# Kernel optimization log

Hardware: AMD Instinct MI355X
Metric: run time of the kernel (lower is better)

Reference implementation:

```python
import jax, jax.numpy as jnp
import numpy as np

N = 100000      # nodes
E = 1600000     # directed edges
F_IN = 128      # node feature dim
H = 128         # hidden dim
C = 16          # classes


def setup_inputs() -> dict:
    key = jax.random.key(0)
    ks = jax.random.split(key, 8)
    s = 1.0 / np.sqrt(H)
    return {
        "x": jax.random.normal(ks[0], (N, F_IN), dtype=jnp.float32),
        "edge_index": jax.random.randint(ks[1], (2, E), 0, N, dtype=jnp.int32),
        "W1": jax.random.normal(ks[2], (F_IN, H), dtype=jnp.float32) * s,
        "b1": jnp.zeros((H,), jnp.float32),
        "W2": jax.random.normal(ks[3], (H, H), dtype=jnp.float32) * s,
        "b2": jnp.zeros((H,), jnp.float32),
        "W3": jax.random.normal(ks[4], (H, H), dtype=jnp.float32) * s,
        "b3": jnp.zeros((H,), jnp.float32),
        "Wfc": jax.random.normal(ks[5], (H, C), dtype=jnp.float32) * s,
        "bfc": jnp.zeros((C,), jnp.float32),
    }


def _gcn_conv(x, W, b, src, dst, norm):
    # x' = b + scatter_add over edges of norm * (x @ W)[src] into dst
    h = x @ W                                   # [N, H] dense GEMM
    msg = h[src] * norm[:, None]                # [E+N, H] gather + scale
    out = jax.ops.segment_sum(msg, dst, num_segments=N)  # scatter-add
    return out + b


def reference(x, edge_index, W1, b1, W2, b2, W3, b3, Wfc, bfc):
    loops = jnp.arange(N, dtype=edge_index.dtype)
    src = jnp.concatenate([edge_index[0], loops])   # [E+N] with self-loops
    dst = jnp.concatenate([edge_index[1], loops])
    # symmetric normalization deg^{-1/2}[src] * deg^{-1/2}[dst] (PyG default)
    deg = jax.ops.segment_sum(jnp.ones_like(dst, dtype=x.dtype), dst, num_segments=N)
    dinv = jax.lax.rsqrt(deg)                       # deg >= 1 due to self-loops
    norm = dinv[src] * dinv[dst]

    h = jax.nn.elu(_gcn_conv(x, W1, b1, src, dst, norm))   # dropout is identity in eval
    h = jax.nn.elu(_gcn_conv(h, W2, b2, src, dst, norm))
    h = jax.nn.elu(_gcn_conv(h, W3, b3, src, dst, norm))
    logits = h @ Wfc + bfc                                  # [N, C]
    return jax.nn.log_softmax(logits, axis=-1)
```

## Files before the change

### kernel.cpp

```cpp
#include <hip/hip_runtime.h>
#include <math.h>

#define HDIM 128
#define CDIM 16
#define CAP 48
#define ASTR 136
#define HSTR 132
#define NBINS 256
#define TILE 4096
#define F2SPLIT 4

typedef unsigned short u16;
typedef unsigned int u32;
typedef __attribute__((ext_vector_type(8))) short short8;
typedef __attribute__((ext_vector_type(4))) float f32x4;
typedef __attribute__((ext_vector_type(2))) float f32x2;

__device__ inline u16 f2bf(float f) {
  u32 u = __float_as_uint(f);
  u += 0x7fffu + ((u >> 16) & 1u);
  return (u16)(u >> 16);
}
__device__ inline float bf_lo(u32 p) { return __uint_as_float(p << 16); }
__device__ inline float bf_hi(u32 p) { return __uint_as_float(p & 0xffff0000u); }
__device__ inline u32 pack2(float a, float b) {
  return (u32)f2bf(a) | ((u32)f2bf(b) << 16);
}
__device__ inline u32 cvtpk(float a, float b) {
  u32 r;
  asm("v_cvt_pk_bf16_f32 %0, %1, %2" : "=v"(r) : "v"(a), "v"(b));
  return r;
}
__device__ inline void acc_word(f32x2& acc, u32 w) {
  f32x2 x;
  x.x = __uint_as_float(w << 16);
  x.y = __uint_as_float(w & 0xffff0000u);
  asm("v_pk_add_f32 %0, %1, %2" : "=v"(acc) : "v"(x), "v"(acc));
}


__global__ __launch_bounds__(256) void bin_kernel(const int* __restrict__ ei,
                                                  int* __restrict__ cursor,
                                                  int2* __restrict__ bins,
                                                  int binCap, int E, int npb, int nbE,
                                                  int* __restrict__ deg, int N,
                                                  const float* __restrict__ W0,
                                                  const float* __restrict__ W1,
                                                  const float* __restrict__ W2,
                                                  u16* __restrict__ Wt) {
  int tid = threadIdx.x;
  if (blockIdx.x >= nbE) {
    int t = (blockIdx.x - nbE) * 256 + tid;
    int which = t >> 14, idx = t & 16383;
    int n = idx >> 7, k = idx & 127;
    const float* W = which == 0 ? W0 : (which == 1 ? W1 : W2);
    Wt[(size_t)which * HDIM * HDIM + n * HDIM + k] = f2bf(W[k * HDIM + n]);
    return;
  }
  {
    int i = blockIdx.x * 256 + tid;
    if (i < N) deg[i] = 0;
  }
  __shared__ int2 eds[TILE];
  __shared__ int base[NBINS], rank[NBINS], hist[NBINS];
  int t0 = blockIdx.x * TILE;
  int n = min(TILE, E - t0);
  for (int i = tid; i < NBINS; i += 256) { hist[i] = 0; rank[i] = 0; }
  __syncthreads();
  for (int i = tid; i < n; i += 256) {
    int s = ei[t0 + i];
    int d = ei[E + t0 + i];
    eds[i] = make_int2(d, s);
    atomicAdd(&hist[d / npb], 1);
  }
  __syncthreads();
  for (int i = tid; i < NBINS; i += 256) {
    int h = hist[i];
    base[i] = h ? atomicAdd(&cursor[i], h) : 0;
  }
  __syncthreads();
  for (int i = tid; i < n; i += 256) {
    int2 e = eds[i];
    int b = e.x / npb;
    int r = base[b] + atomicAdd(&rank[b], 1);
    if (r < binCap) bins[(size_t)b * binCap + r] = e;
  }
}

__global__ __launch_bounds__(256) void fill2_kernel(const int2* __restrict__ bins,
                                                    const int* __restrict__ cursor,
                                                    int binCap, int* __restrict__ deg,
                                                    int* __restrict__ csr) {
  int b = blockIdx.x & (NBINS - 1);
  int part = blockIdx.x >> 8;
  int cnt = min(cursor[b], binCap);
  const int2* eb = bins + (size_t)b * binCap;
  for (int i = part * 256 + threadIdx.x; i < cnt; i += 256 * F2SPLIT) {
    int2 e = eb[i];
    int p = atomicAdd(&deg[e.x], 1);
    if (p < CAP) csr[(size_t)e.x * CAP + p] = e.y;
  }
}

__global__ __launch_bounds__(256) void pad_kernel(const int* __restrict__ deg,
                                                  int* __restrict__ csr, int N) {
  int n = blockIdx.x * 256 + threadIdx.x;
  if (n >= N) return;
  int d = min(deg[n], CAP);
  int dp = (d + 7) & ~7;
  int* row = csr + (size_t)n * CAP;
  for (int i = d; i < dp; ++i) row[i] = N;
}


template <bool FP32IN>
__global__ __launch_bounds__(256) void gemm_k(const void* __restrict__ Xv,
                                              const u16* __restrict__ Wt,
                                              const int* __restrict__ deg,
                                              u16* __restrict__ G, int N) {
  __shared__ u16 As[64 * ASTR];
  __shared__ u16 Wsm[128 * ASTR];
  int tid = threadIdx.x;
  int row0 = blockIdx.x * 64;

  {
    int r = tid >> 2, c = tid & 3;
    int rg = row0 + r;
    if (rg >= N) rg = N - 1;
    uint4* dst = (uint4*)(As + r * ASTR + c * 32);
    if (FP32IN) {
      const float4* src = (const float4*)((const float*)Xv + (size_t)rg * HDIM + c * 32);
#pragma unroll
      for (int j = 0; j < 4; ++j) {
        float4 a = src[2 * j], b = src[2 * j + 1];
        uint4 o;
        o.x = pack2(a.x, a.y); o.y = pack2(a.z, a.w);
        o.z = pack2(b.x, b.y); o.w = pack2(b.z, b.w);
        dst[j] = o;
      }
    } else {
      const uint4* src = (const uint4*)((const u16*)Xv + (size_t)rg * HDIM + c * 32);
      dst[0] = src[0]; dst[1] = src[1]; dst[2] = src[2]; dst[3] = src[3];
    }
  }
  {
    int r = tid >> 1, h = tid & 1;
    const uint4* src = (const uint4*)(Wt + r * HDIM + h * 64);
    uint4* dst = (uint4*)(Wsm + r * ASTR + h * 64);
#pragma unroll
    for (int i = 0; i < 8; ++i) dst[i] = src[i];
  }
  __syncthreads();

  int w = tid >> 6;
  int l = tid & 63;
  int m = l & 15, q = l >> 4;

  f32x4 acc[8];
#pragma unroll
  for (int i = 0; i < 8; ++i) acc[i] = (f32x4){0.f, 0.f, 0.f, 0.f};

#pragma unroll
  for (int kc = 0; kc < 4; ++kc) {
    short8 af = *(const short8*)(As + (w * 16 + m) * ASTR + kc * 32 + q * 8);
#pragma unroll
    for (int nt = 0; nt < 8; ++nt) {
      short8 bfr = *(const short8*)(Wsm + (nt * 16 + m) * ASTR + kc * 32 + q * 8);
      acc[nt] = __builtin_amdgcn_mfma_f32_16x16x32_bf16(af, bfr, acc[nt], 0, 0, 0);
    }
  }
  __syncthreads();

  float dv[4];
#pragma unroll
  for (int r = 0; r < 4; ++r) {
    int rg = row0 + w * 16 + q * 4 + r;
    dv[r] = rsqrtf((float)(deg[rg < N ? rg : N - 1] + 1));
  }
#pragma unroll
  for (int nt = 0; nt < 8; ++nt)
#pragma unroll
    for (int r = 0; r < 4; ++r)
      As[(w * 16 + q * 4 + r) * ASTR + nt * 16 + m] = f2bf(acc[nt][r] * dv[r]);
  __syncthreads();

  {
    int r = tid >> 2, c = tid & 3;
    int rg = row0 + r;
    if (rg < N) {
      uint4* dst = (uint4*)(G + (size_t)rg * HDIM + c * 32);
      const uint4* src = (const uint4*)(As + r * ASTR + c * 32);
      dst[0] = src[0]; dst[1] = src[1]; dst[2] = src[2]; dst[3] = src[3];
    }
  }
}


__device__ inline void gather16(const u16* __restrict__ G, const int* __restrict__ deg,
                                const int* __restrict__ csr,
                                const float4* __restrict__ b4, int node, int l, float* v) {
  const char* Gb = (const char*)G;
  f32x2 p0, p1, p2, p3;
  {
    uint4 sr = *(const uint4*)(Gb + ((size_t)node << 8) + (l << 4));
    p0.x = bf_lo(sr.x); p0.y = bf_hi(sr.x);
    p1.x = bf_lo(sr.y); p1.y = bf_hi(sr.y);
    p2.x = bf_lo(sr.z); p2.y = bf_hi(sr.z);
    p3.x = bf_lo(sr.w); p3.y = bf_hi(sr.w);
  }
  int dfull = deg[node];
  int d = min(dfull, CAP);
  int dp = (d + 7) & ~7;
  const int* row = csr + (size_t)node * CAP;
  int i0 = row[l];
  int i1 = d > 16 ? row[16 + l] : 0;
  int i2 = d > 32 ? row[32 + l] : 0;

#define GLD(u) (*(const uint4*)(Gb + (((u32)(u)) << 8) + (l << 4)))
#define AW(gv) { acc_word(p0, gv.x); acc_word(p1, gv.y); acc_word(p2, gv.z); acc_word(p3, gv.w); }
  for (int k = 0; k < dp; k += 8) {
    int s = k < 16 ? i0 : (k < 32 ? i1 : i2);
    int bl = k & 15;
    int u0 = __shfl(s, bl + 0, 16), u1 = __shfl(s, bl + 1, 16);
    int u2 = __shfl(s, bl + 2, 16), u3 = __shfl(s, bl + 3, 16);
    int u4 = __shfl(s, bl + 4, 16), u5 = __shfl(s, bl + 5, 16);
    int u6 = __shfl(s, bl + 6, 16), u7 = __shfl(s, bl + 7, 16);
    uint4 g0 = GLD(u0), g1 = GLD(u1), g2 = GLD(u2), g3 = GLD(u3);
    uint4 g4 = GLD(u4), g5 = GLD(u5), g6 = GLD(u6), g7 = GLD(u7);
    AW(g0) AW(g1) AW(g2) AW(g3) AW(g4) AW(g5) AW(g6) AW(g7)
  }
#undef AW
#undef GLD
  float dvn = rsqrtf((float)(dfull + 1));
  float4 b0 = b4[l * 2], b1 = b4[l * 2 + 1];
  v[0] = fmaf(dvn, p0.x, b0.x); v[1] = fmaf(dvn, p0.y, b0.y);
  v[2] = fmaf(dvn, p1.x, b0.z); v[3] = fmaf(dvn, p1.y, b0.w);
  v[4] = fmaf(dvn, p2.x, b1.x); v[5] = fmaf(dvn, p2.y, b1.y);
  v[6] = fmaf(dvn, p3.x, b1.z); v[7] = fmaf(dvn, p3.y, b1.w);
#pragma unroll
  for (int j = 0; j < 8; ++j) v[j] = v[j] > 0.f ? v[j] : __expf(v[j]) - 1.f;
}


__global__ __launch_bounds__(256) void agg_gemm(const u16* __restrict__ G,
                                                const int* __restrict__ deg,
                                                const int* __restrict__ csr,
                                                const float* __restrict__ b,
                                                const u16* __restrict__ Wn,
                                                u16* __restrict__ Gout, int N) {
  __shared__ u16 As[16 * ASTR];
  __shared__ float dvs[16];
  int tid = threadIdx.x;
  int node0 = blockIdx.x * 16;
  int lr = tid >> 4, l = tid & 15;
  int node = node0 + lr;
  if (tid < 16) dvs[tid] = rsqrtf((float)(deg[min(node0 + tid, N - 1)] + 1));
  if (node < N) {
    float v[8];
    gather16(G, deg, csr, (const float4*)b, node, l, v);
    uint4 o;
    o.x = cvtpk(v[0], v[1]); o.y = cvtpk(v[2], v[3]);
    o.z = cvtpk(v[4], v[5]); o.w = cvtpk(v[6], v[7]);
    *(uint4*)(As + lr * ASTR + l * 8) = o;
  } else {
    uint4 z = make_uint4(0, 0, 0, 0);
    *(uint4*)(As + lr * ASTR + l * 8) = z;
  }
  __syncthreads();

  int w = tid >> 6;
  int lw = tid & 63;
  int m = lw & 15, q = lw >> 4;
  f32x4 acc0 = (f32x4){0.f, 0.f, 0.f, 0.f};
  f32x4 acc1 = (f32x4){0.f, 0.f, 0.f, 0.f};
#pragma unroll
  for (int kc = 0; kc < 4; ++kc) {
    short8 af = *(const short8*)(As + m * ASTR + kc * 32 + q * 8);
    short8 b0 = *(const short8*)(Wn + ((w * 2 + 0) * 16 + m) * HDIM + kc * 32 + q * 8);
    short8 b1 = *(const short8*)(Wn + ((w * 2 + 1) * 16 + m) * HDIM + kc * 32 + q * 8);
    acc0 = __builtin_amdgcn_mfma_f32_16x16x32_bf16(af, b0, acc0, 0, 0, 0);
    acc1 = __builtin_amdgcn_mfma_f32_16x16x32_bf16(af, b1, acc1, 0, 0, 0);
  }
  __syncthreads();

#pragma unroll
  for (int r = 0; r < 4; ++r) {
    float dvr = dvs[q * 4 + r];
    As[(q * 4 + r) * ASTR + (w * 2 + 0) * 16 + m] = f2bf(acc0[r] * dvr);
    As[(q * 4 + r) * ASTR + (w * 2 + 1) * 16 + m] = f2bf(acc1[r] * dvr);
  }
  __syncthreads();

  {
    int r = tid >> 4, c = tid & 15;
    if (node0 + r < N)
      *(uint4*)(Gout + (size_t)(node0 + r) * HDIM + c * 8) =
          *(const uint4*)(As + r * ASTR + c * 8);
  }
}


__global__ __launch_bounds__(256) void agg_fc(const u16* __restrict__ G,
                                              const int* __restrict__ deg,
                                              const int* __restrict__ csr,
                                              const float* __restrict__ b,
                                              const float* __restrict__ Wfc,
                                              const float* __restrict__ bfc,
                                              float* __restrict__ out, int N) {
  __shared__ float Hs[16 * HSTR];
  __shared__ float Wl[HDIM * CDIM];
  int tid = threadIdx.x;
  for (int i = tid; i < HDIM * CDIM; i += 256) Wl[i] = Wfc[i];

  int node0 = blockIdx.x * 16;
  int lr = tid >> 4, l = tid & 15;
  int node = node0 + lr;
  if (node < N) {
    float v[8];
    gather16(G, deg, csr, (const float4*)b, node, l, v);
    float4* dst = (float4*)(Hs + lr * HSTR + l * 8);
    dst[0] = make_float4(v[0], v[1], v[2], v[3]);
    dst[1] = make_float4(v[4], v[5], v[6], v[7]);
  }
  __syncthreads();

  int rg = node0 + lr;
  if (rg >= N) return;
  int c = l;
  const float* hrow = Hs + lr * HSTR;
  float acc = bfc[c];
#pragma unroll 4
  for (int k4 = 0; k4 < 32; ++k4) {
    float4 g = *(const float4*)(hrow + k4 * 4);
    const float* wk = Wl + (k4 * 4) * CDIM + c;
    acc = fmaf(g.x, wk[0 * CDIM], acc);
    acc = fmaf(g.y, wk[1 * CDIM], acc);
    acc = fmaf(g.z, wk[2 * CDIM], acc);
    acc = fmaf(g.w, wk[3 * CDIM], acc);
  }
  float mx = acc;
  for (int off = 8; off >= 1; off >>= 1) mx = fmaxf(mx, __shfl_xor(mx, off, 16));
  float ex = __expf(acc - mx);
  float ssum = ex;
  for (int off = 8; off >= 1; off >>= 1) ssum += __shfl_xor(ssum, off, 16);
  out[(size_t)rg * CDIM + c] = (acc - mx) - __logf(ssum);
}


extern "C" void kernel_launch(void* const* d_in, const int* in_sizes, int n_in,
                              void* d_out, int out_size, void* d_ws, size_t ws_size,
                              hipStream_t stream) {
  const float* x   = (const float*)d_in[0];
  const int*   ei  = (const int*)d_in[1];
  const float* W1  = (const float*)d_in[2];
  const float* b1  = (const float*)d_in[3];
  const float* W2  = (const float*)d_in[4];
  const float* b2  = (const float*)d_in[5];
  const float* W3  = (const float*)d_in[6];
  const float* b3  = (const float*)d_in[7];
  const float* Wfc = (const float*)d_in[8];
  const float* bfc = (const float*)d_in[9];

  const int N = in_sizes[0] / HDIM;
  const int E = in_sizes[1] / 2;
  const int npb = (N + NBINS - 1) / NBINS;
  const int binCap = (E + NBINS - 1) / NBINS + 1024;
  const int nbE = (E + TILE - 1) / TILE;
  const int nbW = 3 * HDIM * HDIM / 256;

  char* ws = (char*)d_ws;
  size_t off = 0;
  auto alloc = [&](size_t bytes) -> void* {
    void* p = ws + off;
    off += (bytes + 511) & ~(size_t)511;
    return p;
  };
  int*   deg    = (int*)alloc((size_t)N * 4);
  int*   cursor = (int*)alloc((size_t)NBINS * 4);
  int*   csr    = (int*)alloc((size_t)N * CAP * 4);
  int2*  bins   = (int2*)alloc((size_t)NBINS * binCap * 8);
  u16*   Wt     = (u16*)alloc((size_t)3 * HDIM * HDIM * 2);
  u16*   A      = (u16*)alloc((size_t)(N + 1) * HDIM * 2);
  u16*   B      = (u16*)alloc((size_t)(N + 1) * HDIM * 2);

  hipMemsetAsync(cursor, 0, (size_t)NBINS * 4, stream);
  hipMemsetAsync(A + (size_t)N * HDIM, 0, HDIM * 2, stream);
  hipMemsetAsync(B + (size_t)N * HDIM, 0, HDIM * 2, stream);
  bin_kernel<<<nbE + nbW, 256, 0, stream>>>(ei, cursor, bins, binCap, E, npb, nbE, deg, N, W1,
                                            W2, W3, Wt);
  fill2_kernel<<<NBINS * F2SPLIT, 256, 0, stream>>>(bins, cursor, binCap, deg, csr);
  pad_kernel<<<(N + 255) / 256, 256, 0, stream>>>(deg, csr, N);

  int grid64 = (N + 63) / 64;
  int grid16 = (N + 15) / 16;
  gemm_k<true><<<grid64, 256, 0, stream>>>(x, Wt, deg, A, N);
  agg_gemm<<<grid16, 256, 0, stream>>>(A, deg, csr, b1, Wt + HDIM * HDIM, B, N);
  agg_gemm<<<grid16, 256, 0, stream>>>(B, deg, csr, b2, Wt + 2 * HDIM * HDIM, A, N);
  agg_fc<<<grid16, 256, 0, stream>>>(A, deg, csr, b3, Wfc, bfc, (float*)d_out, N);
}
```

Before: 383.0 us.

## Build padded CSR with per-bin shared-memory counting sort, drop pad kernel and memsets

The fill kernel now runs one block per destination bin. Each block does a shared-memory histogram and prefix sum over its nodes, scatters edge sources into a locally sorted buffer, then writes deg and fully padded CSR rows contiguously. This replaces the global per-edge atomics, the separate pad kernel and the deg zeroing. Zeroing of the sentinel rows moves into an extra block of bin_kernel, which removes two memsets and one launch. It risks less parallelism (256 blocks instead of 1024), a serial single-thread prefix scan, and silent truncation if a bin exceeds SORTCAP.

```diff
diff --git a/kernel.cpp b/kernel.cpp
--- a/kernel.cpp
+++ b/kernel.cpp
@@ -8,7 +8,8 @@
 #define HSTR 132
 #define NBINS 256
 #define TILE 4096
-#define F2SPLIT 4
+#define NPBMAX 512
+#define SORTCAP 7424
 
 typedef unsigned short u16;
 typedef unsigned int u32;
@@ -43,13 +44,20 @@
                                                   int* __restrict__ cursor,
                                                   int2* __restrict__ bins,
                                                   int binCap, int E, int npb, int nbE,
-                                                  int* __restrict__ deg, int N,
+                                                  int nbW, int N,
                                                   const float* __restrict__ W0,
                                                   const float* __restrict__ W1,
                                                   const float* __restrict__ W2,
-                                                  u16* __restrict__ Wt) {
+                                                  u16* __restrict__ Wt,
+                                                  u16* __restrict__ Arow,
+                                                  u16* __restrict__ Brow) {
   int tid = threadIdx.x;
   if (blockIdx.x >= nbE) {
+    if (blockIdx.x >= nbE + nbW) {
+      if (tid < 16) ((uint4*)Arow)[tid] = make_uint4(0, 0, 0, 0);
+      else if (tid < 32) ((uint4*)Brow)[tid - 16] = make_uint4(0, 0, 0, 0);
+      return;
+    }
     int t = (blockIdx.x - nbE) * 256 + tid;
     int which = t >> 14, idx = t & 16383;
     int n = idx >> 7, k = idx & 127;
@@ -57,10 +65,6 @@
     Wt[(size_t)which * HDIM * HDIM + n * HDIM + k] = f2bf(W[k * HDIM + n]);
     return;
   }
-  {
-    int i = blockIdx.x * 256 + tid;
-    if (i < N) deg[i] = 0;
-  }
   __shared__ int2 eds[TILE];
   __shared__ int base[NBINS], rank[NBINS], hist[NBINS];
   int t0 = blockIdx.x * TILE;
@@ -89,27 +93,47 @@
 
 __global__ __launch_bounds__(256) void fill2_kernel(const int2* __restrict__ bins,
                                                     const int* __restrict__ cursor,
-                                                    int binCap, int* __restrict__ deg,
-                                                    int* __restrict__ csr) {
-  int b = blockIdx.x & (NBINS - 1);
-  int part = blockIdx.x >> 8;
-  int cnt = min(cursor[b], binCap);
+                                                    int binCap, int npb,
+                                                    int* __restrict__ deg,
+                                                    int* __restrict__ csr, int N) {
+  __shared__ int hist[NPBMAX];
+  __shared__ int base[NPBMAX + 1];
+  __shared__ int sorted[SORTCAP];
+  int b = blockIdx.x;
+  int tid = threadIdx.x;
+  int n0 = b * npb;
+  int nn = min(npb, N - n0);
+  if (nn <= 0) return;
+  int cnt = min(min(cursor[b], binCap), SORTCAP);
   const int2* eb = bins + (size_t)b * binCap;
-  for (int i = part * 256 + threadIdx.x; i < cnt; i += 256 * F2SPLIT) {
+  for (int i = tid; i < nn; i += 256) hist[i] = 0;
+  __syncthreads();
+  for (int i = tid; i < cnt; i += 256) atomicAdd(&hist[eb[i].x - n0], 1);
+  __syncthreads();
+  if (tid == 0) {
+    int s = 0;
+    for (int i = 0; i < nn; ++i) { base[i] = s; s += hist[i]; }
+    base[nn] = s;
+  }
+  __syncthreads();
+  for (int i = tid; i < nn; i += 256) hist[i] = 0;
+  __syncthreads();
+  for (int i = tid; i < cnt; i += 256) {
     int2 e = eb[i];
-    int p = atomicAdd(&deg[e.x], 1);
-    if (p < CAP) csr[(size_t)e.x * CAP + p] = e.y;
-  }
-}
-
-__global__ __launch_bounds__(256) void pad_kernel(const int* __restrict__ deg,
-                                                  int* __restrict__ csr, int N) {
-  int n = blockIdx.x * 256 + threadIdx.x;
-  if (n >= N) return;
-  int d = min(deg[n], CAP);
-  int dp = (d + 7) & ~7;
-  int* row = csr + (size_t)n * CAP;
-  for (int i = d; i < dp; ++i) row[i] = N;
+    int loc = e.x - n0;
+    sorted[base[loc] + atomicAdd(&hist[loc], 1)] = e.y;
+  }
+  __syncthreads();
+  for (int i = tid; i < nn; i += 256) deg[n0 + i] = base[i + 1] - base[i];
+  int total = nn * CAP;
+  int* cout = csr + (size_t)n0 * CAP;
+  for (int i = tid; i < total; i += 256) {
+    int loc = (int)(((u32)(i >> 4) * 21846u) >> 16);
+    int j = i - loc * CAP;
+    int s0 = base[loc];
+    int dc = min(base[loc + 1] - s0, CAP);
+    cout[i] = j < dc ? sorted[s0 + j] : N;
+  }
 }
 
 
@@ -384,12 +408,10 @@
   u16*   B      = (u16*)alloc((size_t)(N + 1) * HDIM * 2);
 
   hipMemsetAsync(cursor, 0, (size_t)NBINS * 4, stream);
-  hipMemsetAsync(A + (size_t)N * HDIM, 0, HDIM * 2, stream);
-  hipMemsetAsync(B + (size_t)N * HDIM, 0, HDIM * 2, stream);
-  bin_kernel<<<nbE + nbW, 256, 0, stream>>>(ei, cursor, bins, binCap, E, npb, nbE, deg, N, W1,
-                                            W2, W3, Wt);
-  fill2_kernel<<<NBINS * F2SPLIT, 256, 0, stream>>>(bins, cursor, binCap, deg, csr);
-  pad_kernel<<<(N + 255) / 256, 256, 0, stream>>>(deg, csr, N);
+  bin_kernel<<<nbE + nbW + 1, 256, 0, stream>>>(ei, cursor, bins, binCap, E, npb, nbE, nbW,
+                                                N, W1, W2, W3, Wt,
+                                                A + (size_t)N * HDIM, B + (size_t)N * HDIM);
+  fill2_kernel<<<NBINS, 256, 0, stream>>>(bins, cursor, binCap, npb, deg, csr, N);
 
   int grid64 = (N + 63) / 64;
   int grid16 = (N + 15) / 16;
```

Measured after the change: 365.9 us. 4.5% less time.
